# Optimization experiments

Measured on AMD Instinct MI355X. Metric: run time of the kernel, lower is better.

Reference implementation:

```python
import jax, jax.numpy as jnp
import numpy as np

N = 50000   # nodes
E = 800000  # edges
IN = 128    # input feature dim
HID = 64    # hidden per head
HEADS = 2
P = 100000  # pos/neg pairs
SLOPE = 0.2 # DGL GATConv default negative_slope
EPS = 1e-5  # BatchNorm eps


def setup_inputs() -> dict:
    key = jax.random.key(0)
    ks = jax.random.split(key, 40)
    nrm = lambda k, s, sc=0.1: jax.random.normal(k, s, jnp.float32) * sc
    inp = {}
    inp['x'] = jax.random.normal(ks[0], (N, IN), jnp.float32)
    inp['edge_src'] = jax.random.randint(ks[1], (E,), 0, N)
    inp['edge_dst'] = jax.random.randint(ks[2], (E,), 0, N)
    inp['pos_src'] = jax.random.randint(ks[3], (P,), 0, N)
    inp['pos_dst'] = jax.random.randint(ks[4], (P,), 0, N)
    inp['neg_src'] = jax.random.randint(ks[5], (P,), 0, N)
    inp['neg_dst'] = jax.random.randint(ks[6], (P,), 0, N)
    # GATConv layer 0: in=IN, out=HID, heads=HEADS
    inp['W0'] = nrm(ks[7], (IN, HEADS * HID))
    inp['al0'] = nrm(ks[8], (HEADS, HID))
    inp['ar0'] = nrm(ks[9], (HEADS, HID))
    inp['b0'] = jnp.zeros((HEADS * HID,), jnp.float32)
    # GATConv layer 1: in=HEADS*HID, out=HID, heads=HEADS
    inp['W1'] = nrm(ks[10], (HEADS * HID, HEADS * HID))
    inp['al1'] = nrm(ks[11], (HEADS, HID))
    inp['ar1'] = nrm(ks[12], (HEADS, HID))
    inp['b1'] = jnp.zeros((HEADS * HID,), jnp.float32)
    # GATConv layer 2: in=HEADS*HID, out=HID, heads=1
    inp['W2'] = nrm(ks[13], (HEADS * HID, HID))
    inp['al2'] = nrm(ks[14], (1, HID))
    inp['ar2'] = nrm(ks[15], (1, HID))
    inp['b2'] = jnp.zeros((HID,), jnp.float32)
    # BatchNorm params
    inp['bn0_g'] = jnp.ones((HEADS * HID,), jnp.float32)
    inp['bn0_b'] = jnp.zeros((HEADS * HID,), jnp.float32)
    inp['bn1_g'] = jnp.ones((HEADS * HID,), jnp.float32)
    inp['bn1_b'] = jnp.zeros((HEADS * HID,), jnp.float32)
    # predictor MLP: HID->HID->HID->1
    inp['pW1'] = nrm(ks[16], (HID, HID))
    inp['pb1'] = jnp.zeros((HID,), jnp.float32)
    inp['pW2'] = nrm(ks[17], (HID, HID))
    inp['pb2'] = jnp.zeros((HID,), jnp.float32)
    inp['pW3'] = nrm(ks[18], (HID, 1))
    inp['pb3'] = jnp.zeros((1,), jnp.float32)
    return inp


def gat_conv(h, src, dst, W, al, ar, b, heads, fh):
    # DGL GATConv: fc -> per-node attn dots -> edge LeakyReLU -> dst-segment softmax -> scatter-add
    feat = (h @ W).reshape(-1, heads, fh)            # [N, H, F]
    el = (feat * al[None]).sum(-1)                   # [N, H]
    er = (feat * ar[None]).sum(-1)                   # [N, H]
    e = jax.nn.leaky_relu(el[src] + er[dst], SLOPE)  # [E, H]
    m = jax.ops.segment_max(e, dst, num_segments=N)  # per-dst max for stability
    ee = jnp.exp(e - m[dst])
    denom = jax.ops.segment_sum(ee, dst, num_segments=N)
    alpha = ee / jnp.maximum(denom[dst], 1e-9)       # [E, H]
    out = jax.ops.segment_sum(alpha[:, :, None] * feat[src], dst, num_segments=N)
    return (out + b.reshape(1, heads, fh)).reshape(-1, heads * fh)


def batch_norm(h, g, b):
    mu = h.mean(0)
    var = jnp.var(h, 0)  # biased, matches torch BN training normalization
    return g * (h - mu) * jax.lax.rsqrt(var + EPS) + b


def predict(h_src, h_dst, pW1, pb1, pW2, pb2, pW3, pb3):
    z = h_src * h_dst
    z = jax.nn.relu(z @ pW1 + pb1)
    z = jax.nn.relu(z @ pW2 + pb2)
    return z @ pW3 + pb3


def reference(x, edge_src, edge_dst, pos_src, pos_dst, neg_src, neg_dst,
              W0, al0, ar0, b0, W1, al1, ar1, b1, W2, al2, ar2, b2,
              bn0_g, bn0_b, bn1_g, bn1_b, pW1, pb1, pW2, pb2, pW3, pb3):
    h = gat_conv(x, edge_src, edge_dst, W0, al0, ar0, b0, HEADS, HID)
    h = jax.nn.relu(batch_norm(h, bn0_g, bn0_b))  # dropout = identity (eval)
    h = gat_conv(h, edge_src, edge_dst, W1, al1, ar1, b1, HEADS, HID)
    h = jax.nn.relu(batch_norm(h, bn1_g, bn1_b))
    h = gat_conv(h, edge_src, edge_dst, W2, al2, ar2, b2, 1, HID)  # [N, HID]
    h_pos = predict(h[pos_src], h[pos_dst], pW1, pb1, pW2, pb2, pW3, pb3)
    h_neg = predict(h[neg_src], h[neg_dst], pW1, pb1, pW2, pb2, pW3, pb3)
    return (h_pos, h_neg)
```

## Files before the change

### kernel.cpp

```cpp
#include <hip/hip_runtime.h>
#include <hip/hip_fp16.h>
#include <cstdint>
#include <cstddef>

#define N_NODES 50000
#define N_EDGES 800000

typedef _Float16 f16x8 __attribute__((ext_vector_type(8)));
typedef float f32x4 __attribute__((ext_vector_type(4)));

__global__ void f32_to_f16(const float* __restrict__ in, __half* __restrict__ outp, int n4)
{
    int i = blockIdx.x * blockDim.x + threadIdx.x;
    int stride = gridDim.x * blockDim.x;
    for (; i < n4; i += stride) {
        float4 v = *reinterpret_cast<const float4*>(in + (size_t)i * 4);
        __half2 a = __floats2half2_rn(v.x, v.y);
        __half2 b = __floats2half2_rn(v.z, v.w);
        uint2 pk;
        pk.x = *reinterpret_cast<unsigned*>(&a);
        pk.y = *reinterpret_cast<unsigned*>(&b);
        *reinterpret_cast<uint2*>(outp + (size_t)i * 4) = pk;
    }
}

__global__ void prep_wt(const float* __restrict__ W0, const float* __restrict__ W1,
                        const float* __restrict__ W2, __half* __restrict__ t0,
                        __half* __restrict__ t1, __half* __restrict__ t2)
{
    int b = blockIdx.x >> 7;
    int k = blockIdx.x & 127;
    int c = threadIdx.x;
    const float* W = (b == 0) ? W0 : (b == 1) ? W1 : W2;
    __half* T = (b == 0) ? t0 : (b == 1) ? t1 : t2;
    int Cb = (b == 2) ? 64 : 128;
    if (c < Cb) T[(size_t)c * 128 + k] = __float2half(W[(size_t)k * Cb + c]);
}

__global__ void prep_pwt(const float* __restrict__ W1, const float* __restrict__ W2,
                         __half* __restrict__ t1, __half* __restrict__ t2)
{
    int b = blockIdx.x >> 6;
    int k = blockIdx.x & 63;
    int c = threadIdx.x;
    const float* W = b ? W2 : W1;
    __half* T = b ? t2 : t1;
    T[(size_t)c * 64 + k] = __float2half(W[(size_t)k * 64 + c]);
}

template <int C, int H>
__launch_bounds__(256, 3)
__global__ void gemm_mfma(const __half* __restrict__ Ah, const __half* __restrict__ Wt,
                          const float* __restrict__ al, const float* __restrict__ ar,
                          __half* __restrict__ feat, float* __restrict__ el,
                          float* __restrict__ er, int n)
{
    constexpr int K = 128;
    constexpr int AS = 136;
    constexpr int CT = C / 16;
    __shared__ __half As[64 * AS];
    __shared__ __half Ws[C * AS];

    const int tid = threadIdx.x;
    const int brow = blockIdx.x * 64;

    for (int idx = tid; idx < 64 * 16; idx += 256) {
        int r = idx >> 4, u = idx & 15;
        int gr = brow + r;
        f16x8 v = {0, 0, 0, 0, 0, 0, 0, 0};
        if (gr < n) v = *reinterpret_cast<const f16x8*>(Ah + (size_t)gr * K + u * 8);
        *reinterpret_cast<f16x8*>(&As[r * AS + u * 8]) = v;
    }
    for (int idx = tid; idx < C * 16; idx += 256) {
        int c = idx >> 4, u = idx & 15;
        *reinterpret_cast<f16x8*>(&Ws[c * AS + u * 8]) =
            *reinterpret_cast<const f16x8*>(Wt + (size_t)c * K + u * 8);
    }
    __syncthreads();

    const int w = tid >> 6;
    const int l = tid & 63;
    const int l15 = l & 15;
    const int kg = l >> 4;

    f32x4 acc[CT];
    #pragma unroll
    for (int ct = 0; ct < CT; ++ct) acc[ct] = (f32x4){0.f, 0.f, 0.f, 0.f};

    #pragma unroll
    for (int kt = 0; kt < 4; ++kt) {
        f16x8 a = *reinterpret_cast<const f16x8*>(&As[(w * 16 + l15) * AS + kt * 32 + kg * 8]);
        #pragma unroll
        for (int ct = 0; ct < CT; ++ct) {
            f16x8 b = *reinterpret_cast<const f16x8*>(&Ws[(ct * 16 + l15) * AS + kt * 32 + kg * 8]);
            acc[ct] = __builtin_amdgcn_mfma_f32_16x16x32_f16(a, b, acc[ct], 0, 0, 0);
        }
    }

    const int row0 = w * 16 + kg * 4;
    float pel[4][H], per_[4][H];
    #pragma unroll
    for (int j = 0; j < 4; ++j)
        #pragma unroll
        for (int h = 0; h < H; ++h) { pel[j][h] = 0.f; per_[j][h] = 0.f; }

    #pragma unroll
    for (int ct = 0; ct < CT; ++ct) {
        int col = ct * 16 + l15;
        int head = (H == 2) ? (col >> 6) : 0;
        int lc = col & 63;
        float av = al[head * 64 + lc];
        float rv = ar[head * 64 + lc];
        #pragma unroll
        for (int j = 0; j < 4; ++j) {
            float fv = acc[ct][j];
            int gr = brow + row0 + j;
            if (gr < n) feat[(size_t)gr * C + col] = __float2half(fv);
            pel[j][head] += fv * av;
            per_[j][head] += fv * rv;
        }
    }
    #pragma unroll
    for (int off = 1; off < 16; off <<= 1) {
        #pragma unroll
        for (int j = 0; j < 4; ++j)
            #pragma unroll
            for (int h = 0; h < H; ++h) {
                pel[j][h] += __shfl_xor(pel[j][h], off, 64);
                per_[j][h] += __shfl_xor(per_[j][h], off, 64);
            }
    }
    if (l15 == 0) {
        #pragma unroll
        for (int j = 0; j < 4; ++j) {
            int gr = brow + row0 + j;
            if (gr < n) {
                if constexpr (H == 2) {
                    float2 e0 = make_float2(pel[j][0], pel[j][1]);
                    float2 e1 = make_float2(per_[j][0], per_[j][1]);
                    *reinterpret_cast<float2*>(el + (size_t)gr * 2) = e0;
                    *reinterpret_cast<float2*>(er + (size_t)gr * 2) = e1;
                } else {
                    el[gr] = pel[j][0];
                    er[gr] = per_[j][0];
                }
            }
        }
    }
}

__global__ void hist_dst(const int* __restrict__ dst, int* __restrict__ cnt, int E)
{
    int base = (blockIdx.x * blockDim.x + threadIdx.x) * 4;
    if (base + 3 < E) {
        int4 d = *reinterpret_cast<const int4*>(dst + base);
        atomicAdd(&cnt[d.x], 1);
        atomicAdd(&cnt[d.y], 1);
        atomicAdd(&cnt[d.z], 1);
        atomicAdd(&cnt[d.w], 1);
    } else {
        for (int e = base; e < E; ++e) atomicAdd(&cnt[dst[e]], 1);
    }
}

__global__ void scan_block_sums(const int* __restrict__ cnt, int* __restrict__ bsum, int n)
{
    __shared__ int sh[256];
    int i = blockIdx.x * 256 + threadIdx.x;
    sh[threadIdx.x] = (i < n) ? cnt[i] : 0;
    __syncthreads();
    for (int off = 128; off; off >>= 1) {
        if (threadIdx.x < off) sh[threadIdx.x] += sh[threadIdx.x + off];
        __syncthreads();
    }
    if (threadIdx.x == 0) bsum[blockIdx.x] = sh[0];
}

__global__ void scan_bsum(int* __restrict__ bsum, int nb)
{
    __shared__ int sh[256];
    int t = threadIdx.x;
    sh[t] = (t < nb) ? bsum[t] : 0;
    __syncthreads();
    for (int off = 1; off < 256; off <<= 1) {
        int u = (t >= off) ? sh[t - off] : 0;
        __syncthreads();
        sh[t] += u;
        __syncthreads();
    }
    if (t < nb) bsum[t] = t ? sh[t - 1] : 0;
}

__global__ void scan_final(const int* __restrict__ cnt, const int* __restrict__ bsum,
                           int* __restrict__ rs, int* __restrict__ cursor, int n)
{
    __shared__ int sh[256];
    int t = threadIdx.x;
    int i = blockIdx.x * 256 + t;
    int v = (i < n) ? cnt[i] : 0;
    sh[t] = v;
    __syncthreads();
    for (int off = 1; off < 256; off <<= 1) {
        int u = (t >= off) ? sh[t - off] : 0;
        __syncthreads();
        sh[t] += u;
        __syncthreads();
    }
    int excl = sh[t] - v + bsum[blockIdx.x];
    if (i < n) { rs[i] = excl; cursor[i] = excl; }
    if (i == n - 1) rs[n] = excl + v;
}

__global__ void scatter_csr(const int* __restrict__ src, const int* __restrict__ dst,
                            int* __restrict__ cursor, int* __restrict__ csr, int E)
{
    int base = (blockIdx.x * blockDim.x + threadIdx.x) * 4;
    if (base + 3 < E) {
        int4 d = *reinterpret_cast<const int4*>(dst + base);
        int4 s = *reinterpret_cast<const int4*>(src + base);
        int p0 = atomicAdd(&cursor[d.x], 1);
        int p1 = atomicAdd(&cursor[d.y], 1);
        int p2 = atomicAdd(&cursor[d.z], 1);
        int p3 = atomicAdd(&cursor[d.w], 1);
        csr[p0] = s.x; csr[p1] = s.y; csr[p2] = s.z; csr[p3] = s.w;
    } else {
        for (int e = base; e < E; ++e) {
            int pos = atomicAdd(&cursor[dst[e]], 1);
            csr[pos] = src[e];
        }
    }
}

template <int C, int H>
__launch_bounds__(256)
__global__ void gat_agg(const int* __restrict__ rs, const int* __restrict__ csr,
                        const float* __restrict__ el, const float* __restrict__ er,
                        const __half* __restrict__ feat, const float* __restrict__ bias,
                        __half* __restrict__ outp, int n)
{
    int node = blockIdx.x * 4 + (threadIdx.x >> 6);
    if (node >= n) return;
    int lane = threadIdx.x & 63;
    int start = rs[node], end = rs[node + 1];

    if constexpr (H == 2) {
        const int slot = lane >> 4;
        const int cl = lane & 15;
        const int h = cl >> 3;
        const float erh = er[(size_t)node * 2 + h];
        float ssum = 0.f;
        float acc[8];
        #pragma unroll
        for (int u = 0; u < 8; ++u) acc[u] = 0.f;
        for (int j = start + slot; j < end; j += 4) {
            int s = csr[j];
            float v = el[(size_t)s * 2 + h] + erh;
            v = v >= 0.f ? v : 0.2f * v;
            float p = __expf(v);
            ssum += p;
            float4 raw = *reinterpret_cast<const float4*>(feat + (size_t)s * C + cl * 8);
            const __half2* hp = reinterpret_cast<const __half2*>(&raw);
            #pragma unroll
            for (int u = 0; u < 4; ++u) {
                float2 f2 = __half22float2(hp[u]);
                acc[2 * u]     = fmaf(p, f2.x, acc[2 * u]);
                acc[2 * u + 1] = fmaf(p, f2.y, acc[2 * u + 1]);
            }
        }
        #pragma unroll
        for (int off = 16; off <= 32; off <<= 1) {
            ssum += __shfl_xor(ssum, off, 64);
            #pragma unroll
            for (int u = 0; u < 8; ++u) acc[u] += __shfl_xor(acc[u], off, 64);
        }
        if (slot == 0) {
            float r = 1.f / fmaxf(ssum, 1e-9f);
            f16x8 o;
            #pragma unroll
            for (int u = 0; u < 8; ++u) o[u] = (_Float16)(acc[u] * r);
            *reinterpret_cast<f16x8*>(outp + (size_t)node * C + cl * 8) = o;
        }
    } else {
        const int slot = lane >> 3;
        const int cl = lane & 7;
        const float er0 = er[node];
        float ssum = 0.f;
        float acc[8];
        #pragma unroll
        for (int u = 0; u < 8; ++u) acc[u] = 0.f;
        for (int j = start + slot; j < end; j += 8) {
            int s = csr[j];
            float v = el[s] + er0;
            v = v >= 0.f ? v : 0.2f * v;
            float p = __expf(v);
            ssum += p;
            float4 raw = *reinterpret_cast<const float4*>(feat + (size_t)s * C + cl * 8);
            const __half2* hp = reinterpret_cast<const __half2*>(&raw);
            #pragma unroll
            for (int u = 0; u < 4; ++u) {
                float2 f2 = __half22float2(hp[u]);
                acc[2 * u]     = fmaf(p, f2.x, acc[2 * u]);
                acc[2 * u + 1] = fmaf(p, f2.y, acc[2 * u + 1]);
            }
        }
        #pragma unroll
        for (int off = 8; off <= 32; off <<= 1) {
            ssum += __shfl_xor(ssum, off, 64);
            #pragma unroll
            for (int u = 0; u < 8; ++u) acc[u] += __shfl_xor(acc[u], off, 64);
        }
        if (slot == 0) {
            float r = 1.f / fmaxf(ssum, 1e-9f);
            f16x8 o;
            #pragma unroll
            for (int u = 0; u < 8; ++u) o[u] = (_Float16)(acc[u] * r + bias[cl * 8 + u]);
            *reinterpret_cast<f16x8*>(outp + (size_t)node * C + cl * 8) = o;
        }
    }
}

__global__ void bn_stats(const __half* __restrict__ h, float* __restrict__ sums, int n)
{
    __shared__ float s1[256], s2[256];
    int c = threadIdx.x & 127, half = threadIdx.x >> 7;
    float ls = 0.f, lq = 0.f;
    for (int r = blockIdx.x * 2 + half; r < n; r += gridDim.x * 2) {
        float v = __half2float(h[(size_t)r * 128 + c]);
        ls += v; lq += v * v;
    }
    s1[threadIdx.x] = ls; s2[threadIdx.x] = lq;
    __syncthreads();
    if (threadIdx.x < 128) {
        atomicAdd(&sums[c], s1[threadIdx.x] + s1[threadIdx.x + 128]);
        atomicAdd(&sums[128 + c], s2[threadIdx.x] + s2[threadIdx.x + 128]);
    }
}

__global__ void bn_apply(const __half* __restrict__ in, __half* __restrict__ outp,
                         const float* __restrict__ sums,
                         const float* __restrict__ g, const float* __restrict__ b,
                         long long npairs)
{
    long long i = (long long)blockIdx.x * blockDim.x + threadIdx.x;
    if (i >= npairs) return;
    int c0 = (int)((i * 2) & 127);
    const float invN = 1.f / (float)N_NODES;
    __half2 v2 = *reinterpret_cast<const __half2*>(in + i * 2);
    float2 v = __half22float2(v2);
    float mean0 = sums[c0] * invN, mean1 = sums[c0 + 1] * invN;
    float var0 = sums[128 + c0] * invN - mean0 * mean0;
    float var1 = sums[128 + c0 + 1] * invN - mean1 * mean1;
    float o0 = fmaxf((v.x - mean0) * rsqrtf(var0 + 1e-5f) * g[c0] + b[c0], 0.f);
    float o1 = fmaxf((v.y - mean1) * rsqrtf(var1 + 1e-5f) * g[c0 + 1] + b[c0 + 1], 0.f);
    *reinterpret_cast<__half2*>(outp + i * 2) = __floats2half2_rn(o0, o1);
}

__launch_bounds__(256, 5)
__global__ void predictor(const __half* __restrict__ h16,
                          const int* __restrict__ ps, const int* __restrict__ pd,
                          const int* __restrict__ ns, const int* __restrict__ nd,
                          const __half* __restrict__ W1t, const float* __restrict__ b1,
                          const __half* __restrict__ W2t, const float* __restrict__ b2,
                          const float* __restrict__ W3, const float* __restrict__ b3,
                          float* __restrict__ out, int P)
{
    constexpr int AS = 72;
    __shared__ __half zt[64 * AS];
    __shared__ __half w1s[64 * AS];
    __shared__ __half w2s[64 * AS];
    const int tid = threadIdx.x;

    for (int idx = tid; idx < 512; idx += 256) {
        int c = idx >> 3, u = idx & 7;
        *reinterpret_cast<f16x8*>(&w1s[c * AS + u * 8]) =
            *reinterpret_cast<const f16x8*>(W1t + (size_t)c * 64 + u * 8);
        *reinterpret_cast<f16x8*>(&w2s[c * AS + u * 8]) =
            *reinterpret_cast<const f16x8*>(W2t + (size_t)c * 64 + u * 8);
    }

    {
        int p = tid >> 2, q = tid & 3;
        int gp = blockIdx.x * 64 + p;
        int s, d;
        if (gp < P) { s = ps[gp]; d = pd[gp]; }
        else        { s = ns[gp - P]; d = nd[gp - P]; }
        const f16x8* hs = reinterpret_cast<const f16x8*>(h16 + (size_t)s * 64 + q * 16);
        const f16x8* hd = reinterpret_cast<const f16x8*>(h16 + (size_t)d * 64 + q * 16);
        #pragma unroll
        for (int u = 0; u < 2; ++u) {
            f16x8 z = hs[u] * hd[u];
            *reinterpret_cast<f16x8*>(&zt[p * AS + q * 16 + u * 8]) = z;
        }
    }
    __syncthreads();

    const int w = tid >> 6;
    const int l = tid & 63;
    const int l15 = l & 15;
    const int kg = l >> 4;
    const int myrow = (w * 16 + l15) * AS;

    f32x4 acc[4];
    {
        f16x8 a0 = *reinterpret_cast<const f16x8*>(&zt[myrow + kg * 8]);
        f16x8 a1 = *reinterpret_cast<const f16x8*>(&zt[myrow + 32 + kg * 8]);
        #pragma unroll
        for (int nt = 0; nt < 4; ++nt) {
            f16x8 b0 = *reinterpret_cast<const f16x8*>(&w1s[(nt * 16 + l15) * AS + kg * 8]);
            f16x8 b1v = *reinterpret_cast<const f16x8*>(&w1s[(nt * 16 + l15) * AS + 32 + kg * 8]);
            acc[nt] = __builtin_amdgcn_mfma_f32_16x16x32_f16(a0, b0, (f32x4){0.f, 0.f, 0.f, 0.f}, 0, 0, 0);
            acc[nt] = __builtin_amdgcn_mfma_f32_16x16x32_f16(a1, b1v, acc[nt], 0, 0, 0);
        }
    }
    {
        #pragma unroll
        for (int nt = 0; nt < 4; ++nt) {
            float bb = b1[nt * 16 + l15];
            #pragma unroll
            for (int j = 0; j < 4; ++j) {
                float v = fmaxf(acc[nt][j] + bb, 0.f);
                zt[(w * 16 + kg * 4 + j) * AS + nt * 16 + l15] = __float2half(v);
            }
        }
    }
    __syncthreads();

    {
        f16x8 a0 = *reinterpret_cast<const f16x8*>(&zt[myrow + kg * 8]);
        f16x8 a1 = *reinterpret_cast<const f16x8*>(&zt[myrow + 32 + kg * 8]);
        #pragma unroll
        for (int nt = 0; nt < 4; ++nt) {
            f16x8 b0 = *reinterpret_cast<const f16x8*>(&w2s[(nt * 16 + l15) * AS + kg * 8]);
            f16x8 b1v = *reinterpret_cast<const f16x8*>(&w2s[(nt * 16 + l15) * AS + 32 + kg * 8]);
            acc[nt] = __builtin_amdgcn_mfma_f32_16x16x32_f16(a0, b0, (f32x4){0.f, 0.f, 0.f, 0.f}, 0, 0, 0);
            acc[nt] = __builtin_amdgcn_mfma_f32_16x16x32_f16(a1, b1v, acc[nt], 0, 0, 0);
        }
    }
    float part[4] = {0.f, 0.f, 0.f, 0.f};
    #pragma unroll
    for (int nt = 0; nt < 4; ++nt) {
        float bb = b2[nt * 16 + l15];
        float wv = W3[nt * 16 + l15];
        #pragma unroll
        for (int j = 0; j < 4; ++j)
            part[j] += fmaxf(acc[nt][j] + bb, 0.f) * wv;
    }
    #pragma unroll
    for (int off = 1; off < 16; off <<= 1) {
        #pragma unroll
        for (int j = 0; j < 4; ++j)
            part[j] += __shfl_xor(part[j], off, 16);
    }
    if (l15 == 0) {
        const float b3v = b3[0];
        int gp0 = blockIdx.x * 64 + w * 16 + kg * 4;
        #pragma unroll
        for (int j = 0; j < 4; ++j)
            out[gp0 + j] = part[j] + b3v;
    }
}

extern "C" void kernel_launch(void* const* d_in, const int* in_sizes, int n_in,
                              void* d_out, int out_size, void* d_ws, size_t ws_size,
                              hipStream_t stream)
{
    const float* x    = (const float*)d_in[0];
    const int* es     = (const int*)d_in[1];
    const int* ed     = (const int*)d_in[2];
    const int* ps     = (const int*)d_in[3];
    const int* pdst   = (const int*)d_in[4];
    const int* ns     = (const int*)d_in[5];
    const int* nd     = (const int*)d_in[6];
    const float* W0   = (const float*)d_in[7];
    const float* al0  = (const float*)d_in[8];
    const float* ar0  = (const float*)d_in[9];
    const float* W1   = (const float*)d_in[11];
    const float* al1  = (const float*)d_in[12];
    const float* ar1  = (const float*)d_in[13];
    const float* W2   = (const float*)d_in[15];
    const float* al2  = (const float*)d_in[16];
    const float* ar2  = (const float*)d_in[17];
    const float* b2   = (const float*)d_in[18];
    const float* bn0g = (const float*)d_in[19];
    const float* bn0b = (const float*)d_in[20];
    const float* bn1g = (const float*)d_in[21];
    const float* bn1b = (const float*)d_in[22];
    const float* pW1  = (const float*)d_in[23];
    const float* pb1  = (const float*)d_in[24];
    const float* pW2  = (const float*)d_in[25];
    const float* pb2  = (const float*)d_in[26];
    const float* pW3  = (const float*)d_in[27];
    const float* pb3  = (const float*)d_in[28];
    float* out = (float*)d_out;

    float* ws = (float*)d_ws;
    size_t off = 0;
    auto alloc = [&](size_t nelem) {
        float* p = ws + off;
        off += (nelem + 63) & ~(size_t)63;
        return p;
    };
    __half* featb = (__half*)alloc((size_t)N_NODES * 64);
    __half* xh    = (__half*)alloc((size_t)N_NODES * 64);
    __half* aggh  = (__half*)alloc((size_t)N_NODES * 64);
    __half* wt0  = (__half*)alloc(128 * 64);
    __half* wt1  = (__half*)alloc(128 * 64);
    __half* wt2  = (__half*)alloc(64 * 64);
    __half* pwt1 = (__half*)alloc(64 * 32);
    __half* pwt2 = (__half*)alloc(64 * 32);
    float* el    = alloc((size_t)N_NODES * 2);
    float* er    = alloc((size_t)N_NODES * 2);
    float* bns   = alloc(256);
    int* cnt     = (int*)alloc(N_NODES);
    int* rs      = (int*)alloc(N_NODES + 1);
    int* cursor  = (int*)alloc(N_NODES);
    int* bsum    = (int*)alloc(256);
    int* csr     = (int*)alloc(N_EDGES);

    dim3 blk(256);
    const int gemmGrid = (N_NODES + 63) / 64;
    const int edge4Grid = (N_EDGES / 4 + 255) / 256;
    const int nodeBlocks = (N_NODES + 255) / 256;
    const int aggGrid = (N_NODES + 3) / 4;
    const long long bnPairs = (long long)N_NODES * 64;

    hipMemsetAsync(cnt, 0, (size_t)N_NODES * sizeof(int), stream);
    hist_dst<<<edge4Grid, blk, 0, stream>>>(ed, cnt, N_EDGES);
    scan_block_sums<<<nodeBlocks, blk, 0, stream>>>(cnt, bsum, N_NODES);
    scan_bsum<<<1, blk, 0, stream>>>(bsum, nodeBlocks);
    scan_final<<<nodeBlocks, blk, 0, stream>>>(cnt, bsum, rs, cursor, N_NODES);
    scatter_csr<<<edge4Grid, blk, 0, stream>>>(es, ed, cursor, csr, N_EDGES);
    f32_to_f16<<<2048, blk, 0, stream>>>(x, xh, N_NODES * 32);
    prep_wt<<<384, dim3(128), 0, stream>>>(W0, W1, W2, wt0, wt1, wt2);
    prep_pwt<<<128, dim3(64), 0, stream>>>(pW1, pW2, pwt1, pwt2);

    gemm_mfma<128, 2><<<gemmGrid, blk, 0, stream>>>(xh, wt0, al0, ar0, featb, el, er, N_NODES);
    gat_agg<128, 2><<<aggGrid, blk, 0, stream>>>(rs, csr, el, er, featb, nullptr, aggh, N_NODES);
    hipMemsetAsync(bns, 0, 256 * sizeof(float), stream);
    bn_stats<<<256, blk, 0, stream>>>(aggh, bns, N_NODES);
    bn_apply<<<(int)((bnPairs + 255) / 256), blk, 0, stream>>>(aggh, xh, bns, bn0g, bn0b, bnPairs);

    gemm_mfma<128, 2><<<gemmGrid, blk, 0, stream>>>(xh, wt1, al1, ar1, featb, el, er, N_NODES);
    gat_agg<128, 2><<<aggGrid, blk, 0, stream>>>(rs, csr, el, er, featb, nullptr, aggh, N_NODES);
    hipMemsetAsync(bns, 0, 256 * sizeof(float), stream);
    bn_stats<<<256, blk, 0, stream>>>(aggh, bns, N_NODES);
    bn_apply<<<(int)((bnPairs + 255) / 256), blk, 0, stream>>>(aggh, xh, bns, bn1g, bn1b, bnPairs);

    gemm_mfma<64, 1><<<gemmGrid, blk, 0, stream>>>(xh, wt2, al2, ar2, featb, el, er, N_NODES);
    gat_agg<64, 1><<<aggGrid, blk, 0, stream>>>(rs, csr, el, er, featb, b2, aggh, N_NODES);

    predictor<<<3125, blk, 0, stream>>>(aggh, ps, pdst, ns, nd,
                                        pwt1, pb1, pwt2, pb2, pW3, pb3, out, 100000);
}
```

Before: 449.7 us.

## Fuse BatchNorm apply into GEMM loads and merge prep kernels into one launch

Removes the separate bn_apply passes by applying BN scale/shift and ReLU while loading A tiles in the next GEMM. The x conversion, weight transposes and memsets are merged into a single prep_all launch, cutting launch overhead and one full read/write of the activations per layer. The histogram and CSR scatter kernels are also changed from four edges per thread to one. Risk: the BN arithmetic now sits inside the GEMM load loop, and the de-vectorized edge kernels issue more, narrower loads.

```diff
diff --git a/kernel.cpp b/kernel.cpp
--- a/kernel.cpp
+++ b/kernel.cpp
@@ -9,49 +9,66 @@
 typedef _Float16 f16x8 __attribute__((ext_vector_type(8)));
 typedef float f32x4 __attribute__((ext_vector_type(4)));
 
-__global__ void f32_to_f16(const float* __restrict__ in, __half* __restrict__ outp, int n4)
-{
-    int i = blockIdx.x * blockDim.x + threadIdx.x;
-    int stride = gridDim.x * blockDim.x;
-    for (; i < n4; i += stride) {
-        float4 v = *reinterpret_cast<const float4*>(in + (size_t)i * 4);
-        __half2 a = __floats2half2_rn(v.x, v.y);
-        __half2 b = __floats2half2_rn(v.z, v.w);
-        uint2 pk;
-        pk.x = *reinterpret_cast<unsigned*>(&a);
-        pk.y = *reinterpret_cast<unsigned*>(&b);
-        *reinterpret_cast<uint2*>(outp + (size_t)i * 4) = pk;
-    }
-}
-
-__global__ void prep_wt(const float* __restrict__ W0, const float* __restrict__ W1,
-                        const float* __restrict__ W2, __half* __restrict__ t0,
-                        __half* __restrict__ t1, __half* __restrict__ t2)
-{
-    int b = blockIdx.x >> 7;
-    int k = blockIdx.x & 127;
-    int c = threadIdx.x;
-    const float* W = (b == 0) ? W0 : (b == 1) ? W1 : W2;
-    __half* T = (b == 0) ? t0 : (b == 1) ? t1 : t2;
-    int Cb = (b == 2) ? 64 : 128;
-    if (c < Cb) T[(size_t)c * 128 + k] = __float2half(W[(size_t)k * Cb + c]);
-}
-
-__global__ void prep_pwt(const float* __restrict__ W1, const float* __restrict__ W2,
-                         __half* __restrict__ t1, __half* __restrict__ t2)
-{
-    int b = blockIdx.x >> 6;
-    int k = blockIdx.x & 63;
-    int c = threadIdx.x;
-    const float* W = b ? W2 : W1;
-    __half* T = b ? t2 : t1;
-    T[(size_t)c * 64 + k] = __float2half(W[(size_t)k * 64 + c]);
-}
-
-template <int C, int H>
+__global__ void prep_all(const float* __restrict__ x, __half* __restrict__ xh,
+                         int* __restrict__ cnt, float* __restrict__ bns,
+                         const float* __restrict__ W0, const float* __restrict__ W1,
+                         const float* __restrict__ W2, __half* __restrict__ t0,
+                         __half* __restrict__ t1, __half* __restrict__ t2,
+                         const float* __restrict__ pW1, const float* __restrict__ pW2,
+                         __half* __restrict__ pt1, __half* __restrict__ pt2)
+{
+    const int b = blockIdx.x;
+    const int tid = threadIdx.x;
+    if (b < 6250) {
+        int i = b * 256 + tid;
+        if (i < N_NODES * 32) {
+            float4 v = *reinterpret_cast<const float4*>(x + (size_t)i * 4);
+            __half2 a = __floats2half2_rn(v.x, v.y);
+            __half2 c = __floats2half2_rn(v.z, v.w);
+            uint2 pk;
+            pk.x = *reinterpret_cast<unsigned*>(&a);
+            pk.y = *reinterpret_cast<unsigned*>(&c);
+            *reinterpret_cast<uint2*>(xh + (size_t)i * 4) = pk;
+        }
+    } else if (b < 6446) {
+        int i = (b - 6250) * 256 + tid;
+        if (i < N_NODES) cnt[i] = 0;
+    } else if (b == 6446) {
+        bns[tid] = 0.f;
+        bns[256 + tid] = 0.f;
+    } else if (b < 6607) {
+        int g = (b - 6447) * 256 + tid;
+        if (g < 16384) {
+            int c = g & 127, k = g >> 7;
+            t0[(size_t)c * 128 + k] = __float2half(W0[(size_t)k * 128 + c]);
+        } else if (g < 32768) {
+            int idx = g - 16384;
+            int c = idx & 127, k = idx >> 7;
+            t1[(size_t)c * 128 + k] = __float2half(W1[(size_t)k * 128 + c]);
+        } else if (g < 40960) {
+            int idx = g - 32768;
+            int c = idx & 63, k = idx >> 6;
+            t2[(size_t)c * 128 + k] = __float2half(W2[(size_t)k * 64 + c]);
+        }
+    } else {
+        int g = (b - 6607) * 256 + tid;
+        if (g < 4096) {
+            int c = g & 63, k = g >> 6;
+            pt1[(size_t)c * 64 + k] = __float2half(pW1[(size_t)k * 64 + c]);
+        } else if (g < 8192) {
+            int idx = g - 4096;
+            int c = idx & 63, k = idx >> 6;
+            pt2[(size_t)c * 64 + k] = __float2half(pW2[(size_t)k * 64 + c]);
+        }
+    }
+}
+
+template <int C, int H, bool BN>
 __launch_bounds__(256, 3)
 __global__ void gemm_mfma(const __half* __restrict__ Ah, const __half* __restrict__ Wt,
                           const float* __restrict__ al, const float* __restrict__ ar,
+                          const float* __restrict__ bns, const float* __restrict__ bng,
+                          const float* __restrict__ bnb,
                           __half* __restrict__ feat, float* __restrict__ el,
                           float* __restrict__ er, int n)
 {
@@ -60,15 +77,36 @@
     constexpr int CT = C / 16;
     __shared__ __half As[64 * AS];
     __shared__ __half Ws[C * AS];
+    __shared__ float sc[128], sh_[128];
 
     const int tid = threadIdx.x;
     const int brow = blockIdx.x * 64;
+
+    if constexpr (BN) {
+        if (tid < 128) {
+            const float invN = 1.f / (float)N_NODES;
+            float mean = bns[tid] * invN;
+            float var = bns[128 + tid] * invN - mean * mean;
+            float s = bng[tid] * rsqrtf(var + 1e-5f);
+            sc[tid] = s;
+            sh_[tid] = bnb[tid] - mean * s;
+        }
+        __syncthreads();
+    }
 
     for (int idx = tid; idx < 64 * 16; idx += 256) {
         int r = idx >> 4, u = idx & 15;
         int gr = brow + r;
         f16x8 v = {0, 0, 0, 0, 0, 0, 0, 0};
         if (gr < n) v = *reinterpret_cast<const f16x8*>(Ah + (size_t)gr * K + u * 8);
+        if constexpr (BN) {
+            #pragma unroll
+            for (int e = 0; e < 8; ++e) {
+                int ch = u * 8 + e;
+                float f = (float)v[e] * sc[ch] + sh_[ch];
+                v[e] = (_Float16)fmaxf(f, 0.f);
+            }
+        }
         *reinterpret_cast<f16x8*>(&As[r * AS + u * 8]) = v;
     }
     for (int idx = tid; idx < C * 16; idx += 256) {
@@ -151,16 +189,8 @@
 
 __global__ void hist_dst(const int* __restrict__ dst, int* __restrict__ cnt, int E)
 {
-    int base = (blockIdx.x * blockDim.x + threadIdx.x) * 4;
-    if (base + 3 < E) {
-        int4 d = *reinterpret_cast<const int4*>(dst + base);
-        atomicAdd(&cnt[d.x], 1);
-        atomicAdd(&cnt[d.y], 1);
-        atomicAdd(&cnt[d.z], 1);
-        atomicAdd(&cnt[d.w], 1);
-    } else {
-        for (int e = base; e < E; ++e) atomicAdd(&cnt[dst[e]], 1);
-    }
+    int e = blockIdx.x * blockDim.x + threadIdx.x;
+    if (e < E) atomicAdd(&cnt[dst[e]], 1);
 }
 
 __global__ void scan_block_sums(const int* __restrict__ cnt, int* __restrict__ bsum, int n)
@@ -214,20 +244,11 @@
 __global__ void scatter_csr(const int* __restrict__ src, const int* __restrict__ dst,
                             int* __restrict__ cursor, int* __restrict__ csr, int E)
 {
-    int base = (blockIdx.x * blockDim.x + threadIdx.x) * 4;
-    if (base + 3 < E) {
-        int4 d = *reinterpret_cast<const int4*>(dst + base);
-        int4 s = *reinterpret_cast<const int4*>(src + base);
-        int p0 = atomicAdd(&cursor[d.x], 1);
-        int p1 = atomicAdd(&cursor[d.y], 1);
-        int p2 = atomicAdd(&cursor[d.z], 1);
-        int p3 = atomicAdd(&cursor[d.w], 1);
-        csr[p0] = s.x; csr[p1] = s.y; csr[p2] = s.z; csr[p3] = s.w;
-    } else {
-        for (int e = base; e < E; ++e) {
-            int pos = atomicAdd(&cursor[dst[e]], 1);
-            csr[pos] = src[e];
-        }
+    int e = blockIdx.x * blockDim.x + threadIdx.x;
+    if (e < E) {
+        int d = dst[e];
+        int pos = atomicAdd(&cursor[d], 1);
+        csr[pos] = src[e];
     }
 }
 
@@ -334,25 +355,6 @@
         atomicAdd(&sums[c], s1[threadIdx.x] + s1[threadIdx.x + 128]);
         atomicAdd(&sums[128 + c], s2[threadIdx.x] + s2[threadIdx.x + 128]);
     }
-}
-
-__global__ void bn_apply(const __half* __restrict__ in, __half* __restrict__ outp,
-                         const float* __restrict__ sums,
-                         const float* __restrict__ g, const float* __restrict__ b,
-                         long long npairs)
-{
-    long long i = (long long)blockIdx.x * blockDim.x + threadIdx.x;
-    if (i >= npairs) return;
-    int c0 = (int)((i * 2) & 127);
-    const float invN = 1.f / (float)N_NODES;
-    __half2 v2 = *reinterpret_cast<const __half2*>(in + i * 2);
-    float2 v = __half22float2(v2);
-    float mean0 = sums[c0] * invN, mean1 = sums[c0 + 1] * invN;
-    float var0 = sums[128 + c0] * invN - mean0 * mean0;
-    float var1 = sums[128 + c0 + 1] * invN - mean1 * mean1;
-    float o0 = fmaxf((v.x - mean0) * rsqrtf(var0 + 1e-5f) * g[c0] + b[c0], 0.f);
-    float o1 = fmaxf((v.y - mean1) * rsqrtf(var1 + 1e-5f) * g[c0 + 1] + b[c0 + 1], 0.f);
-    *reinterpret_cast<__half2*>(outp + i * 2) = __floats2half2_rn(o0, o1);
 }
 
 __launch_bounds__(256, 5)
@@ -510,7 +512,7 @@
     __half* pwt2 = (__half*)alloc(64 * 32);
     float* el    = alloc((size_t)N_NODES * 2);
     float* er    = alloc((size_t)N_NODES * 2);
-    float* bns   = alloc(256);
+    float* bns   = alloc(512);
     int* cnt     = (int*)alloc(N_NODES);
     int* rs      = (int*)alloc(N_NODES + 1);
     int* cursor  = (int*)alloc(N_NODES);
@@ -519,34 +521,30 @@
 
     dim3 blk(256);
     const int gemmGrid = (N_NODES + 63) / 64;
-    const int edge4Grid = (N_EDGES / 4 + 255) / 256;
+    const int edgeGrid = (N_EDGES + 255) / 256;
     const int nodeBlocks = (N_NODES + 255) / 256;
     const int aggGrid = (N_NODES + 3) / 4;
-    const long long bnPairs = (long long)N_NODES * 64;
-
-    hipMemsetAsync(cnt, 0, (size_t)N_NODES * sizeof(int), stream);
-    hist_dst<<<edge4Grid, blk, 0, stream>>>(ed, cnt, N_EDGES);
+
+    prep_all<<<6639, blk, 0, stream>>>(x, xh, cnt, bns, W0, W1, W2, wt0, wt1, wt2,
+                                       pW1, pW2, pwt1, pwt2);
+    hist_dst<<<edgeGrid, blk, 0, stream>>>(ed, cnt, N_EDGES);
     scan_block_sums<<<nodeBlocks, blk, 0, stream>>>(cnt, bsum, N_NODES);
     scan_bsum<<<1, blk, 0, stream>>>(bsum, nodeBlocks);
     scan_final<<<nodeBlocks, blk, 0, stream>>>(cnt, bsum, rs, cursor, N_NODES);
-    scatter_csr<<<edge4Grid, blk, 0, stream>>>(es, ed, cursor, csr, N_EDGES);
-    f32_to_f16<<<2048, blk, 0, stream>>>(x, xh, N_NODES * 32);
-    prep_wt<<<384, dim3(128), 0, stream>>>(W0, W1, W2, wt0, wt1, wt2);
-    prep_pwt<<<128, dim3(64), 0, stream>>>(pW1, pW2, pwt1, pwt2);
-
-    gemm_mfma<128, 2><<<gemmGrid, blk, 0, stream>>>(xh, wt0, al0, ar0, featb, el, er, N_NODES);
+    scatter_csr<<<edgeGrid, blk, 0, stream>>>(es, ed, cursor, csr, N_EDGES);
+
+    gemm_mfma<128, 2, false><<<gemmGrid, blk, 0, stream>>>(xh, wt0, al0, ar0,
+        nullptr, nullptr, nullptr, featb, el, er, N_NODES);
     gat_agg<128, 2><<<aggGrid, blk, 0, stream>>>(rs, csr, el, er, featb, nullptr, aggh, N_NODES);
-    hipMemsetAsync(bns, 0, 256 * sizeof(float), stream);
     bn_stats<<<256, blk, 0, stream>>>(aggh, bns, N_NODES);
-    bn_apply<<<(int)((bnPairs + 255) / 256), blk, 0, stream>>>(aggh, xh, bns, bn0g, bn0b, bnPairs);
-
-    gemm_mfma<128, 2><<<gemmGrid, blk, 0, stream>>>(xh, wt1, al1, ar1, featb, el, er, N_NODES);
+
+    gemm_mfma<128, 2, true><<<gemmGrid, blk, 0, stream>>>(aggh, wt1, al1, ar1,
+        bns, bn0g, bn0b, featb, el, er, N_NODES);
     gat_agg<128, 2><<<aggGrid, blk, 0, stream>>>(rs, csr, el, er, featb, nullptr, aggh, N_NODES);
-    hipMemsetAsync(bns, 0, 256 * sizeof(float), stream);
-    bn_stats<<<256, blk, 0, stream>>>(aggh, bns, N_NODES);
-    bn_apply<<<(int)((bnPairs + 255) / 256), blk, 0, stream>>>(aggh, xh, bns, bn1g, bn1b, bnPairs);
-
-    gemm_mfma<64, 1><<<gemmGrid, blk, 0, stream>>>(xh, wt2, al2, ar2, featb, el, er, N_NODES);
+    bn_stats<<<256, blk, 0, stream>>>(aggh, bns + 256, N_NODES);
+
+    gemm_mfma<64, 1, true><<<gemmGrid, blk, 0, stream>>>(aggh, wt2, al2, ar2,
+        bns + 256, bn1g, bn1b, featb, el, er, N_NODES);
     gat_agg<64, 1><<<aggGrid, blk, 0, stream>>>(rs, csr, el, er, featb, b2, aggh, N_NODES);
 
     predictor<<<3125, blk, 0, stream>>>(aggh, ps, pdst, ns, nd,
```

After: 430.0 us. -4.4%, faster.
